# Performance work log

Hardware: AMD Instinct MI355X
Metric: run time of the kernel (lower is better)

## Reference

```python
import jax, jax.numpy as jnp
import numpy as np

B, P = 8, 768
S = 36                 # sample_points (also deformable offset pairs)
C_IN, C_ADJ = 64, 72   # prior_feat_channels -> adjusted channels
D, G = 512, 4          # fc_hidden_dim, num_groups (= attention heads)
N_OFFSETS, N_STRIPS, DEG = 72, 71, 3


def _bilinear(img, x, y):
    """img: [B,H,W,C]; x,y: [B,N] pixel coords. Bilinear sample, zeros outside."""
    H, W = img.shape[1], img.shape[2]
    x0 = jnp.floor(x); y0 = jnp.floor(y)
    x0i = x0.astype(jnp.int32); y0i = y0.astype(jnp.int32)
    wx1 = x - x0; wy1 = y - y0

    def corner(xi, yi, w):
        valid = (xi >= 0) & (xi < W) & (yi >= 0) & (yi < H)
        xc = jnp.clip(xi, 0, W - 1); yc = jnp.clip(yi, 0, H - 1)
        vals = jax.vmap(lambda f, yy, xx: f[yy, xx])(img, yc, xc)  # [B,N,C]
        return vals * (w * valid)[..., None]

    return (corner(x0i, y0i, (1 - wx1) * (1 - wy1))
            + corner(x0i + 1, y0i, wx1 * (1 - wy1))
            + corner(x0i, y0i + 1, (1 - wx1) * wy1)
            + corner(x0i + 1, y0i + 1, wx1 * wy1))


def _resize_ac(img, Ht, Wt):
    """Bilinear resize with align_corners=True. img: [B,H,W,C]."""
    Bsz, H, W, _ = img.shape
    gy, gx = jnp.meshgrid(jnp.linspace(0.0, H - 1.0, Ht),
                          jnp.linspace(0.0, W - 1.0, Wt), indexing='ij')
    xf = jnp.broadcast_to(gx.reshape(-1), (Bsz, Ht * Wt))
    yf = jnp.broadcast_to(gy.reshape(-1), (Bsz, Ht * Wt))
    return _bilinear(img, xf, yf).reshape(Bsz, Ht, Wt, -1)


def setup_inputs():
    ks = jax.random.split(jax.random.key(0), 32)
    r = lambda i, shp, s=1.0: jax.random.normal(ks[i], shp, dtype=jnp.float32) * s
    z = lambda shp: jnp.zeros(shp, jnp.float32)
    return {
        'feat0': r(0, (B, C_IN, 40, 100)),
        'feat1': r(1, (B, C_IN, 20, 50)),
        'feat2': r(2, (B, C_IN, 10, 25)),
        'priors': jax.random.uniform(ks[3], (B, P, 4 + N_OFFSETS), dtype=jnp.float32) * N_STRIPS,
        'ca_w': r(4, (C_ADJ, C_IN), 0.125), 'ca_b': z((C_ADJ,)),
        'off_w': r(5, (2 * S, C_ADJ), 0.01), 'off_b': r(6, (2 * S,), 0.01),
        'dp_w': r(7, (C_ADJ, C_ADJ), 0.167), 'dp_b': z((C_ADJ,)),
        'z_emb': r(8, (S,), 0.3) + 1.0,
        'gf_w': r(9, (D, S // G, C_ADJ), 0.02), 'gf_b': z((D,)),
        'wq': r(10, (D, D), 0.044), 'bq': z((D,)),
        'wk': r(11, (D, D), 0.044), 'bk': z((D,)),
        'wv': r(12, (D, D), 0.044), 'bv': z((D,)),
        'wo': r(13, (D, D), 0.044), 'bo': z((D,)),
        'cf_w1': r(14, (2 * D, D), 0.044), 'cf_b1': z((2 * D,)),
        'cf_w2': r(15, (D, 2 * D), 0.031), 'cf_b2': z((D,)),
        'cls_w1': r(16, (D, D), 0.044), 'cls_b1': z((D,)),
        'cls_w2': r(17, (2, D), 0.001), 'cls_b2': z((2,)),
        'reg_w1': r(18, (D, D), 0.044), 'reg_b1': z((D,)),
        'p_w1': r(19, (2 * D, D), 0.044), 'p_b1': z((2 * D,)),
        'p_w2': r(20, (DEG + 1, 2 * D), 0.031), 'p_b2': z((DEG + 1,)),
        'b_scale': jnp.ones((1,), jnp.float32), 'b_bias': z((1,)),
    }


def reference(feat0, feat1, feat2, priors, ca_w, ca_b, off_w, off_b, dp_w, dp_b,
              z_emb, gf_w, gf_b, wq, bq, wk, bk, wv, bv, wo, bo,
              cf_w1, cf_b1, cf_w2, cf_b2, cls_w1, cls_b1, cls_w2, cls_b2,
              reg_w1, reg_b1, p_w1, p_b1, p_w2, p_b2, b_scale, b_bias):
    f32 = jnp.float32
    lin = lambda x, w, b: x @ w.T + b

    # ---- prior sampling grid (CLRNet-style) ----
    sx_idx = jnp.floor(jnp.linspace(0.0, 1.0, S) * N_STRIPS).astype(jnp.int32)
    pf_ys = jnp.flip(1.0 - sx_idx.astype(f32) / N_STRIPS)            # [S]
    pf_xs = priors[..., 4 + sx_idx][:, :, ::-1]                       # [B,P,S]
    gx = jnp.clip(pf_xs / N_STRIPS, 0.0, 1.0) * 2.0 - 1.0            # [-1,1]
    gy = jnp.broadcast_to(pf_ys * 2.0 - 1.0, gx.shape)

    # ---- channel adjust (1x1 conv) per level, channels-last ----
    adj = lambda f: jnp.einsum('bchw,oc->bhwo', f, ca_w) + ca_b
    feats = [adj(feat0), adj(feat1), adj(feat2)]                      # [B,H,W,C_ADJ]
    offs0 = jnp.einsum('bhwc,oc->bhwo', feats[0], off_w) + off_b     # [B,H0,W0,2S]

    # ---- deformable multi-level sampling: per (prior, point) gather + 1x1 proj ----
    sidx = jnp.arange(S)
    levels = []
    for l, fl in enumerate(feats):
        Hl, Wl = fl.shape[1], fl.shape[2]
        offs = offs0 if l == 0 else _resize_ac(offs0, Hl, Wl)
        px = (gx + 1.0) * 0.5 * (Wl - 1)
        py = (gy + 1.0) * 0.5 * (Hl - 1)
        ov = _bilinear(offs, px.reshape(B, -1), py.reshape(B, -1)).reshape(B, P, S, S, 2)
        dyx = ov[:, :, sidx, sidx, :]                                 # offset pair s for point s
        sxp = (px + dyx[..., 1]).reshape(B, -1)
        syp = (py + dyx[..., 0]).reshape(B, -1)
        smp = _bilinear(fl, sxp, syp).reshape(B, P, S, C_ADJ)
        levels.append(smp @ dp_w.T + dp_b)
    feat_all = jnp.stack(levels)                                      # [3,B,P,S,C]

    # ---- z-embedding soft level selection ----
    zw = jax.nn.softmax(-(z_emb[:, None] - jnp.arange(3, dtype=f32)) ** 2 / 2.0, axis=-1)  # [S,3]
    feature = jnp.einsum('lbpsc,sl->bpsc', feat_all, zw)

    # ---- grouped gather Conv1d(S -> D, kernel=C_ADJ, groups=G) ----
    xg = feature.reshape(B * P, G, S // G, C_ADJ)
    wg = gf_w.reshape(G, D // G, S // G, C_ADJ)
    feature = (jnp.einsum('ngik,goik->ngo', xg, wg).reshape(B * P, D) + gf_b).reshape(B, P, D)

    # ---- multi-head self-attention over priors + channel MLP residual ----
    dh = D // G
    q = lin(feature, wq, bq).reshape(B, P, G, dh).transpose(0, 2, 1, 3)
    k = lin(feature, wk, bk).reshape(B, P, G, dh).transpose(0, 2, 1, 3)
    v = lin(feature, wv, bv).reshape(B, P, G, dh).transpose(0, 2, 1, 3)
    attn = jax.nn.softmax(jnp.einsum('bgqd,bgkd->bgqk', q, k) / float(np.sqrt(dh)), axis=-1)
    res = jnp.einsum('bgqk,bgkd->bgqd', attn, v).transpose(0, 2, 1, 3).reshape(B, P, D)
    res = lin(res, wo, bo)
    feature = feature + lin(jax.nn.relu(lin(res, cf_w1, cf_b1)), cf_w2, cf_b2)

    # ---- heads ----
    fc = feature.reshape(B * P, D)
    cls_logits = lin(jax.nn.relu(lin(fc, cls_w1, cls_b1)), cls_w2, cls_b2).reshape(B, P, 2)
    reg = jax.nn.relu(lin(fc, reg_w1, reg_b1)).reshape(B, P, D)
    coeffs = lin(jax.nn.relu(lin(reg, p_w1, p_b1)), p_w2, p_b2)       # [B,P,DEG+1]
    coeffs = jnp.concatenate([coeffs[..., :2], coeffs[..., 2:] * b_scale + b_bias], axis=-1)
    ys = jnp.linspace(0.0, 1.0, N_OFFSETS)
    basis = jnp.stack([ys ** i for i in range(DEG + 1)], axis=1)      # [N_OFFSETS, DEG+1]
    xs_pred = jax.nn.sigmoid(jnp.einsum('bnd,od->bno', coeffs, basis))
    return jnp.concatenate([cls_logits, coeffs, xs_pred], axis=-1)    # [B,P,78]
```

## Files before the change

kernel.cpp:

```cpp
#include <hip/hip_runtime.h>
#include <hip/hip_bf16.h>
#include <math.h>

#define BB 8
#define PP 768
#define NPRI 76
#define SS 36
#define CIN 64
#define CADJ 72
#define DD 512

#define H0 40
#define W0 100
#define H1 20
#define W1 50
#define H2 10
#define W2 25

typedef __attribute__((ext_vector_type(8))) short bf16x8;
typedef __attribute__((ext_vector_type(4))) short bf16x4;
typedef __attribute__((ext_vector_type(4))) float f32x4;
#define MFMA_BF16 __builtin_amdgcn_mfma_f32_16x16x32_bf16

typedef const __attribute__((address_space(1))) unsigned int* gas_t;
typedef __attribute__((address_space(3))) unsigned int* las_t;

__device__ __forceinline__ __hip_bfloat16 to_bf16(float v) { return __float2bfloat16(v); }
__device__ __forceinline__ float bf2f(__hip_bfloat16 v) { return __bfloat162float(v); }
__device__ __forceinline__ short to_bf16s(float v) {
    __hip_bfloat16 h = __float2bfloat16(v);
    return *reinterpret_cast<short*>(&h);
}
__device__ __forceinline__ float bfs2f(short s) {
    union { unsigned u; float f; } cv;
    cv.u = ((unsigned)(unsigned short)s) << 16;
    return cv.f;
}

__device__ __forceinline__ float bsample(const float* __restrict__ img, int H, int W,
                                         int C, int c, float x, float y)
{
    float x0f = floorf(x), y0f = floorf(y);
    int x0 = (int)x0f, y0 = (int)y0f;
    float wx1 = x - x0f, wy1 = y - y0f;
    float wx0 = 1.0f - wx1, wy0 = 1.0f - wy1;
    int xc0 = min(max(x0, 0), W - 1);
    int xc1 = min(max(x0 + 1, 0), W - 1);
    int yc0 = min(max(y0, 0), H - 1);
    int yc1 = min(max(y0 + 1, 0), H - 1);
    bool vx0 = (x0 >= 0) && (x0 < W);
    bool vx1 = (x0 + 1 >= 0) && (x0 + 1 < W);
    bool vy0 = (y0 >= 0) && (y0 < H);
    bool vy1 = (y0 + 1 >= 0) && (y0 + 1 < H);
    float w00 = (vx0 && vy0) ? wx0 * wy0 : 0.0f;
    float w01 = (vx1 && vy0) ? wx1 * wy0 : 0.0f;
    float w10 = (vx0 && vy1) ? wx0 * wy1 : 0.0f;
    float w11 = (vx1 && vy1) ? wx1 * wy1 : 0.0f;
    return w00 * img[((size_t)yc0 * W + xc0) * C + c]
         + w01 * img[((size_t)yc0 * W + xc1) * C + c]
         + w10 * img[((size_t)yc1 * W + xc0) * C + c]
         + w11 * img[((size_t)yc1 * W + xc1) * C + c];
}

__global__ __launch_bounds__(256) void k_wprep(
    const float* __restrict__ wq, const float* __restrict__ wk, const float* __restrict__ wv,
    const float* __restrict__ wo, const float* __restrict__ cf_w1, const float* __restrict__ cf_w2,
    const float* __restrict__ cls_w1, const float* __restrict__ reg_w1, const float* __restrict__ p_w1,
    const float* __restrict__ bq, const float* __restrict__ bk, const float* __restrict__ bv,
    const float* __restrict__ cls_b1, const float* __restrict__ reg_b1,
    const float* __restrict__ gf_w, const float* __restrict__ dp_w,
    const float* __restrict__ dp_b, const float* __restrict__ gf_b,
    __hip_bfloat16* __restrict__ wqkv, __hip_bfloat16* __restrict__ wo_bf,
    __hip_bfloat16* __restrict__ cf1_bf, __hip_bfloat16* __restrict__ cf2_bf,
    __hip_bfloat16* __restrict__ clsreg_bf, __hip_bfloat16* __restrict__ p1_bf,
    __hip_bfloat16* __restrict__ gfw2, float* __restrict__ b2,
    float* __restrict__ bqkv, float* __restrict__ bclsreg)
{
    __shared__ float dpS[CADJ][CADJ + 1];
    __shared__ float gfr[648];
    const int bid = blockIdx.x;
    const int tid = threadIdx.x;

    if (bid < 512) {
        const int o = bid;
        for (int i = tid; i < CADJ * CADJ; i += 256) dpS[i / CADJ][i % CADJ] = dp_w[i];
        for (int i = tid; i < 648; i += 256) gfr[i] = gf_w[(size_t)o * 648 + i];
        __syncthreads();
        for (int t = tid; t < 672; t += 256) {
            float acc = 0.0f;
            if (t < 648) {
                const int i = t / 72, m = t % 72;
                const float* gr = gfr + i * 72;
#pragma unroll 8
                for (int k = 0; k < 72; ++k) acc = fmaf(gr[k], dpS[k][m], acc);
            }
            gfw2[(size_t)o * 672 + t] = to_bf16(acc);
        }
        return;
    }
    if (bid < 514) {
        const int o = (bid - 512) * 256 + tid;
        if (o < DD) {
            const float* gr = gf_w + (size_t)o * 648;
            float acc = gf_b[o];
            for (int j = 0; j < 648; ++j) acc = fmaf(gr[j], dp_b[j % 72], acc);
            b2[o] = acc;
        }
        return;
    }
    long i = (long)(bid - 514) * 256 + tid;
    if (i < 262144) { wqkv[i] = to_bf16(wq[i]); return; }
    i -= 262144;
    if (i < 262144) { wqkv[262144 + i] = to_bf16(wk[i]); return; }
    i -= 262144;
    if (i < 262144) { wqkv[524288 + i] = to_bf16(wv[i]); return; }
    i -= 262144;
    if (i < 262144) { wo_bf[i] = to_bf16(wo[i]); return; }
    i -= 262144;
    if (i < 524288) { cf1_bf[i] = to_bf16(cf_w1[i]); return; }
    i -= 524288;
    if (i < 524288) { cf2_bf[i] = to_bf16(cf_w2[i]); return; }
    i -= 524288;
    if (i < 262144) { clsreg_bf[i] = to_bf16(cls_w1[i]); return; }
    i -= 262144;
    if (i < 262144) { clsreg_bf[262144 + i] = to_bf16(reg_w1[i]); return; }
    i -= 262144;
    if (i < 524288) { p1_bf[i] = to_bf16(p_w1[i]); return; }
    i -= 524288;
    if (i < 512) { bqkv[i] = bq[i]; return; }
    if (i < 1024) { bqkv[i] = bk[i - 512]; return; }
    if (i < 1536) { bqkv[i] = bv[i - 1024]; return; }
    i -= 1536;
    if (i < 512) { bclsreg[i] = cls_b1[i]; return; }
    if (i < 1024) { bclsreg[i] = reg_b1[i - 512]; return; }
}

__global__ __launch_bounds__(256) void k_adjoff(
    const float* __restrict__ f, const float* __restrict__ caw, const float* __restrict__ cab,
    const float* __restrict__ offw, const float* __restrict__ offb,
    __hip_bfloat16* __restrict__ feout, float* __restrict__ offout, int HW, int do_off)
{
    __shared__ float inS[64][65];
    __shared__ float wS[72][64];
    __shared__ float owS[72][73];
    __shared__ float feS[64][73];
    __shared__ float cabS[72], obS[72];

    const int tid = threadIdx.x;
    const int b = blockIdx.y;
    const int pix0 = blockIdx.x * 64;
    const int cnt = min(64, HW - pix0);
    const int px = tid & 63, og = tid >> 6, o0 = og * 18;

    const float* fb = f + (size_t)b * CIN * HW + pix0;
    for (int i = tid; i < 72 * 64; i += 256) wS[i >> 6][i & 63] = caw[i];
    if (do_off)
        for (int i = tid; i < 72 * 72; i += 256) owS[i / 72][i % 72] = offw[i];
    if (tid < 72) { cabS[tid] = cab[tid]; obS[tid] = do_off ? offb[tid] : 0.f; }
    for (int i = tid; i < 64 * 64; i += 256) {
        const int c = i >> 6, p = i & 63;
        inS[c][p] = (p < cnt) ? fb[(size_t)c * HW + p] : 0.f;
    }
    __syncthreads();

    float acc[18];
#pragma unroll
    for (int j = 0; j < 18; ++j) acc[j] = cabS[o0 + j];
#pragma unroll 4
    for (int c = 0; c < 64; ++c) {
        const float v = inS[c][px];
#pragma unroll
        for (int j = 0; j < 18; ++j) acc[j] = fmaf(v, wS[o0 + j][c], acc[j]);
    }
#pragma unroll
    for (int j = 0; j < 18; ++j) feS[px][o0 + j] = acc[j];
    __syncthreads();

    __hip_bfloat16* feg = feout + ((size_t)b * HW + pix0) * CADJ;
    for (int i = tid; i < cnt * CADJ; i += 256) feg[i] = to_bf16(feS[i / CADJ][i % CADJ]);

    if (!do_off) return;

    float acc2[18];
#pragma unroll
    for (int j = 0; j < 18; ++j) acc2[j] = obS[o0 + j];
#pragma unroll 4
    for (int c = 0; c < 72; ++c) {
        const float v = feS[px][c];
#pragma unroll
        for (int j = 0; j < 18; ++j) acc2[j] = fmaf(v, owS[o0 + j][c], acc2[j]);
    }
    __syncthreads();
#pragma unroll
    for (int j = 0; j < 18; ++j) feS[px][o0 + j] = acc2[j];
    __syncthreads();
    float* ofg = offout + ((size_t)b * HW + pix0) * CADJ;
    for (int i = tid; i < cnt * CADJ; i += 256) ofg[i] = feS[i / CADJ][i % CADJ];
}

__global__ __launch_bounds__(256) void k_adj12(
    const float* __restrict__ f1, const float* __restrict__ f2,
    const float* __restrict__ caw, const float* __restrict__ cab,
    __hip_bfloat16* __restrict__ fe1, __hip_bfloat16* __restrict__ fe2)
{
    __shared__ float inS[64][65];
    __shared__ float wS[72][64];
    __shared__ float feS[64][73];
    __shared__ float cabS[72];

    const int tid = threadIdx.x;
    const int b = blockIdx.y;
    const int bx = blockIdx.x;
    const float* f;
    __hip_bfloat16* fe;
    int HW, pix0;
    if (bx < 16) { f = f1; fe = fe1; HW = H1 * W1; pix0 = bx * 64; }
    else         { f = f2; fe = fe2; HW = H2 * W2; pix0 = (bx - 16) * 64; }
    const int cnt = min(64, HW - pix0);
    const int px = tid & 63, og = tid >> 6, o0 = og * 18;

    const float* fb = f + (size_t)b * CIN * HW + pix0;
    for (int i = tid; i < 72 * 64; i += 256) wS[i >> 6][i & 63] = caw[i];
    if (tid < 72) cabS[tid] = cab[tid];
    for (int i = tid; i < 64 * 64; i += 256) {
        const int c = i >> 6, p = i & 63;
        inS[c][p] = (p < cnt) ? fb[(size_t)c * HW + p] : 0.f;
    }
    __syncthreads();

    float acc[18];
#pragma unroll
    for (int j = 0; j < 18; ++j) acc[j] = cabS[o0 + j];
#pragma unroll 4
    for (int c = 0; c < 64; ++c) {
        const float v = inS[c][px];
#pragma unroll
        for (int j = 0; j < 18; ++j) acc[j] = fmaf(v, wS[o0 + j][c], acc[j]);
    }
#pragma unroll
    for (int j = 0; j < 18; ++j) feS[px][o0 + j] = acc[j];
    __syncthreads();

    __hip_bfloat16* feg = fe + ((size_t)b * HW + pix0) * CADJ;
    for (int i = tid; i < cnt * CADJ; i += 256) feg[i] = to_bf16(feS[i / CADJ][i % CADJ]);
}

__global__ __launch_bounds__(256) void k_resize2(const float* __restrict__ src,
    float* __restrict__ of1, float* __restrict__ of2)
{
    const int T1 = BB * H1 * W1 * CADJ;
    const int T2 = BB * H2 * W2 * CADJ;
    int idx = blockIdx.x * 256 + threadIdx.x;
    if (idx < T1) {
        const int c = idx % CADJ;
        const int j = (idx / CADJ) % W1;
        const int i = (idx / (CADJ * W1)) % H1;
        const int b = idx / (CADJ * W1 * H1);
        float sy = fminf((float)i * ((float)(H0 - 1) / (float)(H1 - 1)), (float)(H0 - 1));
        float sx = fminf((float)j * ((float)(W0 - 1) / (float)(W1 - 1)), (float)(W0 - 1));
        of1[idx] = bsample(src + (size_t)b * H0 * W0 * CADJ, H0, W0, CADJ, c, sx, sy);
        return;
    }
    idx -= T1;
    if (idx >= T2) return;
    const int c = idx % CADJ;
    const int j = (idx / CADJ) % W2;
    const int i = (idx / (CADJ * W2)) % H2;
    const int b = idx / (CADJ * W2 * H2);
    float sy = fminf((float)i * ((float)(H0 - 1) / (float)(H2 - 1)), (float)(H0 - 1));
    float sx = fminf((float)j * ((float)(W0 - 1) / (float)(W2 - 1)), (float)(W0 - 1));
    of2[idx] = bsample(src + (size_t)b * H0 * W0 * CADJ, H0, W0, CADJ, c, sx, sy);
}

__global__ __launch_bounds__(256) void k_sample(
    const float* __restrict__ priors,
    const __hip_bfloat16* __restrict__ feats0, const __hip_bfloat16* __restrict__ feats1,
    const __hip_bfloat16* __restrict__ feats2,
    const float* __restrict__ offs0,  const float* __restrict__ offs1,  const float* __restrict__ offs2,
    const float* __restrict__ z_emb,
    __hip_bfloat16* __restrict__ fsout)
{
    const int bid = blockIdx.x;
    const int gi = (bid & 7) * 384 + (bid >> 3);
    const int bp0 = gi * 2;
    const int b = bp0 / PP;
    const int tid = threadIdx.x;

    __shared__ __align__(16) int   ib[2][3][SS][4];
    __shared__ __align__(16) float wz[2][3][SS][4];

    const int Hs[3] = {H0, H1, H2};
    const int Wsz[3] = {W0, W1, W2};
    const __hip_bfloat16* Fb[3] = { feats0 + (size_t)b * H0 * W0 * CADJ,
                                    feats1 + (size_t)b * H1 * W1 * CADJ,
                                    feats2 + (size_t)b * H2 * W2 * CADJ };
    const float* Ob[3] = { offs0 + (size_t)b * H0 * W0 * CADJ,
                           offs1 + (size_t)b * H1 * W1 * CADJ,
                           offs2 + (size_t)b * H2 * W2 * CADJ };

    if (tid < 2 * 3 * SS) {
        const int p = tid / 108;
        const int l = (tid % 108) / SS;
        const int s = tid % SS;
        const int bp = bp0 + p;
        const float t = (float)(35 - s) / 35.0f;
        const int m = (int)floorf(t * 71.0f);
        const float pfx = priors[(size_t)bp * NPRI + 4 + m];
        const float gxv = fminf(fmaxf(pfx / 71.0f, 0.0f), 1.0f) * 2.0f - 1.0f;
        const float gyv = (1.0f - (float)m / 71.0f) * 2.0f - 1.0f;
        const float z = z_emb[s];
        const float e0 = expf(-0.5f * z * z);
        const float e1 = expf(-0.5f * (z - 1.0f) * (z - 1.0f));
        const float e2 = expf(-0.5f * (z - 2.0f) * (z - 2.0f));
        const float inv = 1.0f / (e0 + e1 + e2);
        const float ev[3] = {e0, e1, e2};
        const float zwl = ev[l] * inv;

        const int Hl = Hs[l], Wl = Wsz[l];
        const float px = (gxv + 1.0f) * 0.5f * (float)(Wl - 1);
        const float py = (gyv + 1.0f) * 0.5f * (float)(Hl - 1);
        const float dy = bsample(Ob[l], Hl, Wl, CADJ, 2 * s,     px, py);
        const float dx = bsample(Ob[l], Hl, Wl, CADJ, 2 * s + 1, px, py);
        const float sx = px + dx, sy = py + dy;
        const float x0f = floorf(sx), y0f = floorf(sy);
        const int x0 = (int)x0f, y0 = (int)y0f;
        const float wx1 = sx - x0f, wy1 = sy - y0f;
        const float wx0 = 1.0f - wx1, wy0 = 1.0f - wy1;
        const bool vx0 = (x0 >= 0) && (x0 < Wl);
        const bool vx1 = (x0 + 1 >= 0) && (x0 + 1 < Wl);
        const bool vy0 = (y0 >= 0) && (y0 < Hl);
        const bool vy1 = (y0 + 1 >= 0) && (y0 + 1 < Hl);
        const int xc0 = min(max(x0, 0), Wl - 1);
        const int xc1 = min(max(x0 + 1, 0), Wl - 1);
        const int yc0 = min(max(y0, 0), Hl - 1);
        const int yc1 = min(max(y0 + 1, 0), Hl - 1);
        wz[p][l][s][0] = ((vx0 && vy0) ? wx0 * wy0 : 0.0f) * zwl;
        wz[p][l][s][1] = ((vx1 && vy0) ? wx1 * wy0 : 0.0f) * zwl;
        wz[p][l][s][2] = ((vx0 && vy1) ? wx0 * wy1 : 0.0f) * zwl;
        wz[p][l][s][3] = ((vx1 && vy1) ? wx1 * wy1 : 0.0f) * zwl;
        ib[p][l][s][0] = (yc0 * Wl + xc0) * CADJ;
        ib[p][l][s][1] = (yc0 * Wl + xc1) * CADJ;
        ib[p][l][s][2] = (yc1 * Wl + xc0) * CADJ;
        ib[p][l][s][3] = (yc1 * Wl + xc1) * CADJ;
    }
    __syncthreads();

    for (int idx = tid; idx < 2 * SS * 18; idx += 256) {
        const int p = idx / 648;
        const int rem = idx % 648;
        const int s = rem / 18, k4 = (rem % 18) * 4;
        float a0 = 0.f, a1 = 0.f, a2 = 0.f, a3 = 0.f;
#pragma unroll
        for (int l = 0; l < 3; ++l) {
            const __hip_bfloat16* F = Fb[l];
            const int4   i4 = *(const int4*)&ib[p][l][s][0];
            const float4 w4 = *(const float4*)&wz[p][l][s][0];
            const bf16x4 v0 = *(const bf16x4*)(F + i4.x + k4);
            const bf16x4 v1 = *(const bf16x4*)(F + i4.y + k4);
            const bf16x4 v2 = *(const bf16x4*)(F + i4.z + k4);
            const bf16x4 v3 = *(const bf16x4*)(F + i4.w + k4);
            a0 = fmaf(w4.x, bfs2f(v0[0]), a0); a1 = fmaf(w4.x, bfs2f(v0[1]), a1);
            a2 = fmaf(w4.x, bfs2f(v0[2]), a2); a3 = fmaf(w4.x, bfs2f(v0[3]), a3);
            a0 = fmaf(w4.y, bfs2f(v1[0]), a0); a1 = fmaf(w4.y, bfs2f(v1[1]), a1);
            a2 = fmaf(w4.y, bfs2f(v1[2]), a2); a3 = fmaf(w4.y, bfs2f(v1[3]), a3);
            a0 = fmaf(w4.z, bfs2f(v2[0]), a0); a1 = fmaf(w4.z, bfs2f(v2[1]), a1);
            a2 = fmaf(w4.z, bfs2f(v2[2]), a2); a3 = fmaf(w4.z, bfs2f(v2[3]), a3);
            a0 = fmaf(w4.w, bfs2f(v3[0]), a0); a1 = fmaf(w4.w, bfs2f(v3[1]), a1);
            a2 = fmaf(w4.w, bfs2f(v3[2]), a2); a3 = fmaf(w4.w, bfs2f(v3[3]), a3);
        }
        bf16x4 pk;
        pk[0] = to_bf16s(a0); pk[1] = to_bf16s(a1);
        pk[2] = to_bf16s(a2); pk[3] = to_bf16s(a3);
        __hip_bfloat16* orow = fsout + (size_t)(bp0 + p) * 2688;
        *(bf16x4*)&orow[(s / 9) * 672 + (s % 9) * 72 + k4] = pk;
    }
    if (tid < 2 * 96) {
        const int p = tid / 96, g = (tid % 96) / 24, t = tid % 24;
        fsout[(size_t)(bp0 + p) * 2688 + g * 672 + 648 + t] = to_bf16(0.0f);
    }
}

__global__ __launch_bounds__(256) void k_bgemm(
    const __hip_bfloat16* __restrict__ A, int lda, long sAz,
    const __hip_bfloat16* __restrict__ W, int ldw, long sWz,
    const float* __restrict__ bias, int sBz,
    const __hip_bfloat16* __restrict__ Res, int ldres,
    __hip_bfloat16* __restrict__ C, int ldc, int sCz,
    int K, int relu)
{
    __shared__ __hip_bfloat16 As[2][128][32];
    __shared__ __hip_bfloat16 Bs[2][128][32];
    const int tid = threadIdx.x;
    const int lane = tid & 63, w = tid >> 6;
    const int wr = w >> 1, wc = w & 1;
    const int row16 = lane & 15, kg = lane >> 4;
    const int z = blockIdx.z;
    const int m0 = blockIdx.y * 128, n0 = blockIdx.x * 128;
    const __hip_bfloat16* Ab = A + (size_t)z * sAz;
    const __hip_bfloat16* Wb = W + (size_t)z * sWz;
    const int gr = lane >> 2;
    const int gc = (lane & 3) * 8;

#define STAGE128(buf, kbase)                                                       \
    {                                                                              \
        _Pragma("unroll")                                                          \
        for (int c = 0; c < 2; ++c) {                                              \
            const int r = w * 32 + c * 16;                                         \
            __builtin_amdgcn_global_load_lds(                                      \
                (gas_t)(Ab + (size_t)(m0 + r + gr) * lda + (kbase) + gc),          \
                (las_t)&As[buf][r][0], 16, 0, 0);                                  \
            __builtin_amdgcn_global_load_lds(                                      \
                (gas_t)(Wb + (size_t)(n0 + r + gr) * ldw + (kbase) + gc),          \
                (las_t)&Bs[buf][r][0], 16, 0, 0);                                  \
        }                                                                          \
    }

    f32x4 acc[4][4];
#pragma unroll
    for (int i = 0; i < 4; ++i)
#pragma unroll
        for (int j = 0; j < 4; ++j) acc[i][j] = (f32x4){0.f, 0.f, 0.f, 0.f};

    STAGE128(0, 0)
    __syncthreads();

    int cur = 0;
    for (int k0 = 0; k0 < K; k0 += 32) {
        if (k0 + 32 < K) STAGE128(cur ^ 1, k0 + 32)
        bf16x8 af[4], bfr[4];
#pragma unroll
        for (int i = 0; i < 4; ++i) af[i]  = *(const bf16x8*)&As[cur][wr * 64 + i * 16 + row16][kg * 8];
#pragma unroll
        for (int j = 0; j < 4; ++j) bfr[j] = *(const bf16x8*)&Bs[cur][wc * 64 + j * 16 + row16][kg * 8];
#pragma unroll
        for (int i = 0; i < 4; ++i)
#pragma unroll
            for (int j = 0; j < 4; ++j)
                acc[i][j] = MFMA_BF16(af[i], bfr[j], acc[i][j], 0, 0, 0);
        __syncthreads();
        cur ^= 1;
    }
#undef STAGE128

    const float* bz = bias + (size_t)z * sBz;
    __hip_bfloat16* Cz = C + (size_t)z * sCz;
#pragma unroll
    for (int i = 0; i < 4; ++i) {
#pragma unroll
        for (int r = 0; r < 4; ++r) {
            const int row = m0 + wr * 64 + i * 16 + kg * 4 + r;
#pragma unroll
            for (int j = 0; j < 4; ++j) {
                const int col = n0 + wc * 64 + j * 16 + row16;
                float v = acc[i][j][r] + bz[col];
                if (Res) v += bf2f(Res[(size_t)row * ldres + col]);
                if (relu) v = fmaxf(v, 0.0f);
                Cz[(size_t)row * ldc + col] = to_bf16(v);
            }
        }
    }
}

__global__ __launch_bounds__(256) void k_bgemm64(
    const __hip_bfloat16* __restrict__ A, int lda, long sAz,
    const __hip_bfloat16* __restrict__ W, int ldw, long sWz,
    const float* __restrict__ bias, int sBz,
    const __hip_bfloat16* __restrict__ Res, int ldres,
    __hip_bfloat16* __restrict__ C, int ldc, int sCz,
    int K, int relu)
{
    __shared__ __hip_bfloat16 As[2][64][32];
    __shared__ __hip_bfloat16 Bs[2][64][32];
    const int tid = threadIdx.x;
    const int lane = tid & 63, w = tid >> 6;
    const int wr = w >> 1, wc = w & 1;
    const int row16 = lane & 15, kg = lane >> 4;
    const int z = blockIdx.z;
    const int m0 = blockIdx.y * 64, n0 = blockIdx.x * 64;
    const __hip_bfloat16* Ab = A + (size_t)z * sAz;
    const __hip_bfloat16* Wb = W + (size_t)z * sWz;
    const int gr = lane >> 2;
    const int gc = (lane & 3) * 8;

    f32x4 acc[2][2];
#pragma unroll
    for (int i = 0; i < 2; ++i)
#pragma unroll
        for (int j = 0; j < 2; ++j) acc[i][j] = (f32x4){0.f, 0.f, 0.f, 0.f};

    __builtin_amdgcn_global_load_lds(
        (gas_t)(Ab + (size_t)(m0 + w * 16 + gr) * lda + gc),
        (las_t)&As[0][w * 16][0], 16, 0, 0);
    __builtin_amdgcn_global_load_lds(
        (gas_t)(Wb + (size_t)(n0 + w * 16 + gr) * ldw + gc),
        (las_t)&Bs[0][w * 16][0], 16, 0, 0);
    __syncthreads();

    int cur = 0;
    for (int k0 = 0; k0 < K; k0 += 32) {
        if (k0 + 32 < K) {
            const int nxt = cur ^ 1;
            __builtin_amdgcn_global_load_lds(
                (gas_t)(Ab + (size_t)(m0 + w * 16 + gr) * lda + k0 + 32 + gc),
                (las_t)&As[nxt][w * 16][0], 16, 0, 0);
            __builtin_amdgcn_global_load_lds(
                (gas_t)(Wb + (size_t)(n0 + w * 16 + gr) * ldw + k0 + 32 + gc),
                (las_t)&Bs[nxt][w * 16][0], 16, 0, 0);
        }
        bf16x8 af[2], bfr[2];
#pragma unroll
        for (int i = 0; i < 2; ++i) af[i]  = *(const bf16x8*)&As[cur][wr * 32 + i * 16 + row16][kg * 8];
#pragma unroll
        for (int j = 0; j < 2; ++j) bfr[j] = *(const bf16x8*)&Bs[cur][wc * 32 + j * 16 + row16][kg * 8];
#pragma unroll
        for (int i = 0; i < 2; ++i)
#pragma unroll
            for (int j = 0; j < 2; ++j)
                acc[i][j] = MFMA_BF16(af[i], bfr[j], acc[i][j], 0, 0, 0);
        __syncthreads();
        cur ^= 1;
    }

    const float* bz = bias + (size_t)z * sBz;
    __hip_bfloat16* Cz = C + (size_t)z * sCz;
#pragma unroll
    for (int i = 0; i < 2; ++i) {
#pragma unroll
        for (int r = 0; r < 4; ++r) {
            const int row = m0 + wr * 32 + i * 16 + kg * 4 + r;
#pragma unroll
            for (int j = 0; j < 2; ++j) {
                const int col = n0 + wc * 32 + j * 16 + row16;
                float v = acc[i][j][r] + bz[col];
                if (Res) v += bf2f(Res[(size_t)row * ldres + col]);
                if (relu) v = fmaxf(v, 0.0f);
                Cz[(size_t)row * ldc + col] = to_bf16(v);
            }
        }
    }
}

__global__ __launch_bounds__(256) void k_vt(
    const __hip_bfloat16* __restrict__ qkv, __hip_bfloat16* __restrict__ Vt)
{
    const int kt = blockIdx.x;
    const int bg = blockIdx.y;
    const int b = bg >> 2, g = bg & 3;
    const int tid = threadIdx.x;
    __shared__ unsigned short Vs[64][130];

    const __hip_bfloat16* src = qkv + (size_t)(b * PP + kt * 64) * 1536 + 1024 + g * 128;
    for (int i = tid; i < 1024; i += 256) {
        const int row = i >> 4, ch = i & 15;
        *(bf16x8*)&Vs[row][ch * 8] = *(const bf16x8*)(src + (size_t)row * 1536 + ch * 8);
    }
    __syncthreads();
    __hip_bfloat16* dst = Vt + (size_t)bg * 128 * 768 + kt * 64;
    for (int i = tid; i < 1024; i += 256) {
        const int d = i >> 3, kc = i & 7;
        bf16x8 pk;
#pragma unroll
        for (int j = 0; j < 8; ++j) pk[j] = (short)Vs[kc * 8 + j][d];
        *(bf16x8*)(dst + (size_t)d * 768 + kc * 8) = pk;
    }
}

__global__ __launch_bounds__(256) void k_fattn(
    const __hip_bfloat16* __restrict__ qkv, const __hip_bfloat16* __restrict__ Vt,
    __hip_bfloat16* __restrict__ Out)
{
    const int id = blockIdx.x;
    const int xcd = id & 7, rest = id >> 3;
    const int bg = xcd * 4 + rest / 12;
    const int qt = rest % 12;
    const int b = bg >> 2, g = bg & 3;
    const int tid = threadIdx.x, lane = tid & 63, w = tid >> 6;
    const int row16 = lane & 15, kg = lane >> 4;
    const int q0 = qt * 64;

    __shared__ __hip_bfloat16 Klds[64][136];
    __shared__ __hip_bfloat16 Vtl[128][72];
    __shared__ __hip_bfloat16 Plds[4][16][72];

    const size_t rowQ = (size_t)(b * PP + q0 + w * 16 + row16) * 1536 + g * 128;
    bf16x8 aq[4];
#pragma unroll
    for (int t = 0; t < 4; ++t)
        aq[t] = *(const bf16x8*)(qkv + rowQ + t * 32 + kg * 8);

    f32x4 oacc[8];
#pragma unroll
    for (int dt = 0; dt < 8; ++dt) oacc[dt] = (f32x4){0.f, 0.f, 0.f, 0.f};
    float mrow[4] = {-3.0e38f, -3.0e38f, -3.0e38f, -3.0e38f};
    float lrow[4] = {0.f, 0.f, 0.f, 0.f};

    const __hip_bfloat16* Kb = qkv + (size_t)(b * PP) * 1536 + 512 + g * 128;
    const __hip_bfloat16* Vb = Vt + (size_t)bg * 128 * 768;
    const float sc = 0.08838834764831845f;

    const int krow = tid >> 2, kch = tid & 3;
    const int vrow = tid >> 1, vch = tid & 1;
    bf16x8 kreg[4], vreg[4];

    {
        const __hip_bfloat16* s1 = Kb + (size_t)krow * 1536 + kch * 32;
        const __hip_bfloat16* s2 = Vb + (size_t)vrow * 768 + vch * 32;
#pragma unroll
        for (int j = 0; j < 4; ++j) { kreg[j] = *(const bf16x8*)(s1 + j * 8);
                                      vreg[j] = *(const bf16x8*)(s2 + j * 8); }
    }

    for (int kt = 0; kt < 12; ++kt) {
        __syncthreads();
#pragma unroll
        for (int j = 0; j < 4; ++j) {
            *(bf16x8*)&Klds[krow][kch * 32 + j * 8] = kreg[j];
            *(bf16x8*)&Vtl[vrow][vch * 32 + j * 8] = vreg[j];
        }
        __syncthreads();
        if (kt < 11) {
            const __hip_bfloat16* s1 = Kb + (size_t)((kt + 1) * 64 + krow) * 1536 + kch * 32;
            const __hip_bfloat16* s2 = Vb + (size_t)vrow * 768 + (kt + 1) * 64 + vch * 32;
#pragma unroll
            for (int j = 0; j < 4; ++j) { kreg[j] = *(const bf16x8*)(s1 + j * 8);
                                          vreg[j] = *(const bf16x8*)(s2 + j * 8); }
        }

        f32x4 s4[4];
#pragma unroll
        for (int st = 0; st < 4; ++st) s4[st] = (f32x4){0.f, 0.f, 0.f, 0.f};
        __builtin_amdgcn_s_setprio(1);
#pragma unroll
        for (int st = 0; st < 4; ++st)
#pragma unroll
            for (int t = 0; t < 4; ++t)
                s4[st] = MFMA_BF16(aq[t],
                    *(const bf16x8*)&Klds[st * 16 + row16][t * 32 + kg * 8], s4[st], 0, 0, 0);
        __builtin_amdgcn_s_setprio(0);

        float pm[4];
#pragma unroll
        for (int r = 0; r < 4; ++r) {
            float m0 = fmaxf(fmaxf(s4[0][r], s4[1][r]), fmaxf(s4[2][r], s4[3][r])) * sc;
            m0 = fmaxf(m0, __shfl_xor(m0, 1));
            m0 = fmaxf(m0, __shfl_xor(m0, 2));
            m0 = fmaxf(m0, __shfl_xor(m0, 4));
            m0 = fmaxf(m0, __shfl_xor(m0, 8));
            pm[r] = m0;
        }
        const float need = fmaxf(fmaxf(pm[0] - mrow[0], pm[1] - mrow[1]),
                                 fmaxf(pm[2] - mrow[2], pm[3] - mrow[3]));
        if (!__all(need <= 8.0f)) {
#pragma unroll
            for (int r = 0; r < 4; ++r) {
                const float mn = fmaxf(mrow[r], pm[r]);
                const float so = __expf(mrow[r] - mn);
                lrow[r] *= so;
#pragma unroll
                for (int dt = 0; dt < 8; ++dt) oacc[dt][r] *= so;
                mrow[r] = mn;
            }
        }
#pragma unroll
        for (int r = 0; r < 4; ++r) {
            float rs = 0.f;
#pragma unroll
            for (int st = 0; st < 4; ++st) {
                const float p = __expf(s4[st][r] * sc - mrow[r]);
                rs += p;
                Plds[w][kg * 4 + r][st * 16 + row16] = to_bf16(p);
            }
            rs += __shfl_xor(rs, 1);
            rs += __shfl_xor(rs, 2);
            rs += __shfl_xor(rs, 4);
            rs += __shfl_xor(rs, 8);
            lrow[r] += rs;
        }

        __builtin_amdgcn_s_setprio(1);
#pragma unroll
        for (int ks = 0; ks < 2; ++ks) {
            bf16x8 ap = *(const bf16x8*)&Plds[w][row16][ks * 32 + kg * 8];
#pragma unroll
            for (int dt = 0; dt < 8; ++dt)
                oacc[dt] = MFMA_BF16(ap,
                    *(const bf16x8*)&Vtl[dt * 16 + row16][ks * 32 + kg * 8], oacc[dt], 0, 0, 0);
        }
        __builtin_amdgcn_s_setprio(0);
    }

    const size_t obase = (size_t)(b * PP + q0 + w * 16 + kg * 4) * DD + g * 128;
#pragma unroll
    for (int r = 0; r < 4; ++r) {
        const float inv = 1.0f / lrow[r];
#pragma unroll
        for (int dt = 0; dt < 8; ++dt)
            Out[obase + (size_t)r * DD + dt * 16 + row16] = to_bf16(oacc[dt][r] * inv);
    }
}

__global__ __launch_bounds__(64) void k_head(
    const __hip_bfloat16* __restrict__ clsreg, const __hip_bfloat16* __restrict__ ph,
    const float* __restrict__ cls_w2, const float* __restrict__ cls_b2,
    const float* __restrict__ p_w2, const float* __restrict__ p_b2,
    const float* __restrict__ b_scale, const float* __restrict__ b_bias,
    float* __restrict__ outp)
{
    const int bp = blockIdx.x;
    const int lane = threadIdx.x;
    const __hip_bfloat16* hr = clsreg + (size_t)bp * 1024;
    float a0 = 0.0f, a1 = 0.0f;
    for (int i = lane; i < DD; i += 64) {
        float h = bf2f(hr[i]);
        a0 = fmaf(h, cls_w2[i], a0);
        a1 = fmaf(h, cls_w2[DD + i], a1);
    }
    const __hip_bfloat16* pr = ph + (size_t)bp * 1024;
    float c0 = 0.0f, c1 = 0.0f, c2 = 0.0f, c3 = 0.0f;
    for (int i = lane; i < 1024; i += 64) {
        float h = bf2f(pr[i]);
        c0 = fmaf(h, p_w2[i], c0);
        c1 = fmaf(h, p_w2[1024 + i], c1);
        c2 = fmaf(h, p_w2[2048 + i], c2);
        c3 = fmaf(h, p_w2[3072 + i], c3);
    }
#pragma unroll
    for (int off = 32; off > 0; off >>= 1) {
        a0 += __shfl_down(a0, off);
        a1 += __shfl_down(a1, off);
        c0 += __shfl_down(c0, off);
        c1 += __shfl_down(c1, off);
        c2 += __shfl_down(c2, off);
        c3 += __shfl_down(c3, off);
    }
    a0 = __shfl(a0, 0); a1 = __shfl(a1, 0);
    c0 = __shfl(c0, 0); c1 = __shfl(c1, 0);
    c2 = __shfl(c2, 0); c3 = __shfl(c3, 0);
    const float k0 = c0 + p_b2[0];
    const float k1 = c1 + p_b2[1];
    const float scv = b_scale[0], biv = b_bias[0];
    const float k2 = (c2 + p_b2[2]) * scv + biv;
    const float k3 = (c3 + p_b2[3]) * scv + biv;
    float* orow = outp + (size_t)bp * 78;
    if (lane == 0) {
        orow[0] = a0 + cls_b2[0];
        orow[1] = a1 + cls_b2[1];
        orow[2] = k0; orow[3] = k1; orow[4] = k2; orow[5] = k3;
    }
    for (int o = lane; o < 72; o += 64) {
        float ys = (float)o / 71.0f;
        float tv = k0 + ys * (k1 + ys * (k2 + ys * k3));
        orow[6 + o] = 1.0f / (1.0f + expf(-tv));
    }
}

extern "C" void kernel_launch(void* const* d_in, const int* in_sizes, int n_in,
                              void* d_out, int out_size, void* d_ws, size_t ws_size,
                              hipStream_t stream)
{
    const float* feat0  = (const float*)d_in[0];
    const float* feat1  = (const float*)d_in[1];
    const float* feat2  = (const float*)d_in[2];
    const float* priors = (const float*)d_in[3];
    const float* ca_w   = (const float*)d_in[4];
    const float* ca_b   = (const float*)d_in[5];
    const float* off_w  = (const float*)d_in[6];
    const float* off_b  = (const float*)d_in[7];
    const float* dp_w   = (const float*)d_in[8];
    const float* dp_b   = (const float*)d_in[9];
    const float* z_emb  = (const float*)d_in[10];
    const float* gf_w   = (const float*)d_in[11];
    const float* gf_b   = (const float*)d_in[12];
    const float* wq     = (const float*)d_in[13];
    const float* bq     = (const float*)d_in[14];
    const float* wk     = (const float*)d_in[15];
    const float* bk     = (const float*)d_in[16];
    const float* wv     = (const float*)d_in[17];
    const float* bv     = (const float*)d_in[18];
    const float* wo     = (const float*)d_in[19];
    const float* bo     = (const float*)d_in[20];
    const float* cf_w1  = (const float*)d_in[21];
    const float* cf_b1  = (const float*)d_in[22];
    const float* cf_w2  = (const float*)d_in[23];
    const float* cf_b2  = (const float*)d_in[24];
    const float* cls_w1 = (const float*)d_in[25];
    const float* cls_b1 = (const float*)d_in[26];
    const float* cls_w2 = (const float*)d_in[27];
    const float* cls_b2 = (const float*)d_in[28];
    const float* reg_w1 = (const float*)d_in[29];
    const float* reg_b1 = (const float*)d_in[30];
    const float* p_w1   = (const float*)d_in[31];
    const float* p_b1   = (const float*)d_in[32];
    const float* p_w2   = (const float*)d_in[33];
    const float* p_b2   = (const float*)d_in[34];
    const float* b_scale = (const float*)d_in[35];
    const float* b_bias  = (const float*)d_in[36];
    float* out = (float*)d_out;

    char* wsb = (char*)d_ws;
    __hip_bfloat16* feature = (__hip_bfloat16*)(wsb + 0);
    __hip_bfloat16* qkvb    = (__hip_bfloat16*)(wsb + 6291456);
    __hip_bfloat16* tb      = (__hip_bfloat16*)(wsb + 25165824);
    __hip_bfloat16* vtb     = (__hip_bfloat16*)(wsb + 31457280);
    __hip_bfloat16* rb      = (__hip_bfloat16*)(wsb + 31457280);
    __hip_bfloat16* hb      = (__hip_bfloat16*)(wsb + 37748736);
    __hip_bfloat16* f2      = (__hip_bfloat16*)(wsb + 50331648);
    __hip_bfloat16* clsregb = (__hip_bfloat16*)(wsb + 56623104);
    __hip_bfloat16* phb     = (__hip_bfloat16*)(wsb + 69206016);
    float* of1 = (float*)(wsb + 6291456);
    float* of2 = (float*)(wsb + 8595456);
    __hip_bfloat16* fe1 = (__hip_bfloat16*)(wsb + 9171456);
    __hip_bfloat16* fe2 = (__hip_bfloat16*)(wsb + 11475456);
    __hip_bfloat16* fsb = (__hip_bfloat16*)(wsb + 25165824);
    __hip_bfloat16* fe0 = (__hip_bfloat16*)(wsb + 58195968);
    float* of0 = (float*)(wsb + 67411968);
    __hip_bfloat16* wqkv_bf   = (__hip_bfloat16*)(wsb + 81788928);
    __hip_bfloat16* wo_bf     = (__hip_bfloat16*)(wsb + 83361792);
    __hip_bfloat16* cf1_bf    = (__hip_bfloat16*)(wsb + 83886080);
    __hip_bfloat16* cf2_bf    = (__hip_bfloat16*)(wsb + 84934656);
    __hip_bfloat16* clsreg_bf = (__hip_bfloat16*)(wsb + 85983232);
    __hip_bfloat16* p1_bf     = (__hip_bfloat16*)(wsb + 87031808);
    __hip_bfloat16* gfw2_bf   = (__hip_bfloat16*)(wsb + 88080384);
    float* bqkv    = (float*)(wsb + 88768512);
    float* bclsreg = (float*)(wsb + 88774656);
    float* b2      = (float*)(wsb + 88778752);

    k_wprep<<<12812, 256, 0, stream>>>(
        wq, wk, wv, wo, cf_w1, cf_w2, cls_w1, reg_w1, p_w1, bq, bk, bv, cls_b1, reg_b1,
        gf_w, dp_w, dp_b, gf_b,
        wqkv_bf, wo_bf, cf1_bf, cf2_bf, clsreg_bf, p1_bf, gfw2_bf, b2, bqkv, bclsreg);

    k_adjoff<<<dim3(63, BB), 256, 0, stream>>>(feat0, ca_w, ca_b, off_w, off_b,
                                               fe0, of0, H0 * W0, 1);
    k_adj12<<<dim3(20, BB), 256, 0, stream>>>(feat1, feat2, ca_w, ca_b, fe1, fe2);
    k_resize2<<<(BB * (H1 * W1 + H2 * W2) * CADJ + 255) / 256, 256, 0, stream>>>(of0, of1, of2);
    k_sample<<<3072, 256, 0, stream>>>(priors, fe0, fe1, fe2, of0, of1, of2, z_emb, fsb);

    const int M = BB * PP;
    k_bgemm64<<<dim3(2, M / 64, 4), 256, 0, stream>>>(
        fsb, 2688, 672, gfw2_bf, 672, 128 * 672, b2, 128,
        nullptr, 0, feature, DD, 128, 672, 0);
    k_bgemm<<<dim3(12, M / 128, 1), 256, 0, stream>>>(
        feature, DD, 0, wqkv_bf, DD, 0, bqkv, 0,
        nullptr, 0, qkvb, 1536, 0, DD, 0);
    k_vt<<<dim3(12, 32), 256, 0, stream>>>(qkvb, vtb);
    k_fattn<<<384, 256, 0, stream>>>(qkvb, vtb, tb);
    k_bgemm64<<<dim3(8, M / 64, 1), 256, 0, stream>>>(
        tb, DD, 0, wo_bf, DD, 0, bo, 0, nullptr, 0, rb, DD, 0, DD, 0);
    k_bgemm64<<<dim3(16, M / 64, 1), 256, 0, stream>>>(
        rb, DD, 0, cf1_bf, DD, 0, cf_b1, 0, nullptr, 0, hb, 1024, 0, DD, 1);
    k_bgemm64<<<dim3(8, M / 64, 1), 256, 0, stream>>>(
        hb, 1024, 0, cf2_bf, 1024, 0, cf_b2, 0, feature, DD, f2, DD, 0, 1024, 0);
    k_bgemm64<<<dim3(16, M / 64, 1), 256, 0, stream>>>(
        f2, DD, 0, clsreg_bf, DD, 0, bclsreg, 0, nullptr, 0, clsregb, 1024, 0, DD, 1);
    k_bgemm64<<<dim3(16, M / 64, 1), 256, 0, stream>>>(
        clsregb + 512, 1024, 0, p1_bf, DD, 0, p_b1, 0, nullptr, 0, phb, 1024, 0, DD, 1);

    k_head<<<M, 64, 0, stream>>>(clsregb, phb, cls_w2, cls_b2, p_w2, p_b2, b_scale, b_bias, out);
}
```

Measured before the change: 284.9 us.

## Vectorize weight casts, merge adj12 with resize, batch head and sample work

The weight-prep kernel now casts four floats per thread with float4 loads and packed bf16 stores, which cuts its grid about fourfold, and a single block copies the biases. The level-1/2 channel-adjust kernel and the offset resize kernel are merged into one launch. Each sample thread now handles both priors of a block, so index math is shared and more loads are in flight. The head kernel packs four rows per 256-thread block. The merge reads of0, written by an earlier launch on the same stream, so ordering is kept, but the cuts are mostly launch and overhead savings on small kernels.

```diff
diff --git a/kernel.cpp b/kernel.cpp
--- a/kernel.cpp
+++ b/kernel.cpp
@@ -62,6 +62,15 @@
          + w11 * img[((size_t)yc1 * W + xc1) * C + c];
 }
 
+__device__ __forceinline__ void cast4(__hip_bfloat16* dst, const float* src, long i)
+{
+    const float4 v = *(const float4*)(src + i * 4);
+    bf16x4 pk;
+    pk[0] = to_bf16s(v.x); pk[1] = to_bf16s(v.y);
+    pk[2] = to_bf16s(v.z); pk[3] = to_bf16s(v.w);
+    *(bf16x4*)(dst + i * 4) = pk;
+}
+
 __global__ __launch_bounds__(256) void k_wprep(
     const float* __restrict__ wq, const float* __restrict__ wk, const float* __restrict__ wv,
     const float* __restrict__ wo, const float* __restrict__ cf_w1, const float* __restrict__ cf_w2,
@@ -108,31 +117,34 @@
         }
         return;
     }
-    long i = (long)(bid - 514) * 256 + tid;
-    if (i < 262144) { wqkv[i] = to_bf16(wq[i]); return; }
-    i -= 262144;
-    if (i < 262144) { wqkv[262144 + i] = to_bf16(wk[i]); return; }
-    i -= 262144;
-    if (i < 262144) { wqkv[524288 + i] = to_bf16(wv[i]); return; }
-    i -= 262144;
-    if (i < 262144) { wo_bf[i] = to_bf16(wo[i]); return; }
-    i -= 262144;
-    if (i < 524288) { cf1_bf[i] = to_bf16(cf_w1[i]); return; }
-    i -= 524288;
-    if (i < 524288) { cf2_bf[i] = to_bf16(cf_w2[i]); return; }
-    i -= 524288;
-    if (i < 262144) { clsreg_bf[i] = to_bf16(cls_w1[i]); return; }
-    i -= 262144;
-    if (i < 262144) { clsreg_bf[262144 + i] = to_bf16(reg_w1[i]); return; }
-    i -= 262144;
-    if (i < 524288) { p1_bf[i] = to_bf16(p_w1[i]); return; }
-    i -= 524288;
-    if (i < 512) { bqkv[i] = bq[i]; return; }
-    if (i < 1024) { bqkv[i] = bk[i - 512]; return; }
-    if (i < 1536) { bqkv[i] = bv[i - 1024]; return; }
-    i -= 1536;
-    if (i < 512) { bclsreg[i] = cls_b1[i]; return; }
-    if (i < 1024) { bclsreg[i] = reg_b1[i - 512]; return; }
+    if (bid < 3586) {
+        long i = (long)(bid - 514) * 256 + tid;
+        if (i < 65536) { cast4(wqkv, wq, i); return; }
+        i -= 65536;
+        if (i < 65536) { cast4(wqkv + 262144, wk, i); return; }
+        i -= 65536;
+        if (i < 65536) { cast4(wqkv + 524288, wv, i); return; }
+        i -= 65536;
+        if (i < 65536) { cast4(wo_bf, wo, i); return; }
+        i -= 65536;
+        if (i < 131072) { cast4(cf1_bf, cf_w1, i); return; }
+        i -= 131072;
+        if (i < 131072) { cast4(cf2_bf, cf_w2, i); return; }
+        i -= 131072;
+        if (i < 65536) { cast4(clsreg_bf, cls_w1, i); return; }
+        i -= 65536;
+        if (i < 65536) { cast4(clsreg_bf + 262144, reg_w1, i); return; }
+        i -= 65536;
+        if (i < 131072) { cast4(p1_bf, p_w1, i); return; }
+        return;
+    }
+    for (int i = tid; i < 2560; i += 256) {
+        if (i < 512) bqkv[i] = bq[i];
+        else if (i < 1024) bqkv[i] = bk[i - 512];
+        else if (i < 1536) bqkv[i] = bv[i - 1024];
+        else if (i < 2048) bclsreg[i - 1536] = cls_b1[i - 1536];
+        else bclsreg[i - 1536] = reg_b1[i - 2048];
+    }
 }
 
 __global__ __launch_bounds__(256) void k_adjoff(
@@ -198,59 +210,61 @@
     for (int i = tid; i < cnt * CADJ; i += 256) ofg[i] = feS[i / CADJ][i % CADJ];
 }
 
-__global__ __launch_bounds__(256) void k_adj12(
+__global__ __launch_bounds__(256) void k_adjr12(
     const float* __restrict__ f1, const float* __restrict__ f2,
     const float* __restrict__ caw, const float* __restrict__ cab,
-    __hip_bfloat16* __restrict__ fe1, __hip_bfloat16* __restrict__ fe2)
-{
-    __shared__ float inS[64][65];
-    __shared__ float wS[72][64];
-    __shared__ float feS[64][73];
-    __shared__ float cabS[72];
-
+    __hip_bfloat16* __restrict__ fe1, __hip_bfloat16* __restrict__ fe2,
+    const float* __restrict__ of0, float* __restrict__ of1, float* __restrict__ of2)
+{
+    const int blk = blockIdx.x;
     const int tid = threadIdx.x;
-    const int b = blockIdx.y;
-    const int bx = blockIdx.x;
-    const float* f;
-    __hip_bfloat16* fe;
-    int HW, pix0;
-    if (bx < 16) { f = f1; fe = fe1; HW = H1 * W1; pix0 = bx * 64; }
-    else         { f = f2; fe = fe2; HW = H2 * W2; pix0 = (bx - 16) * 64; }
-    const int cnt = min(64, HW - pix0);
-    const int px = tid & 63, og = tid >> 6, o0 = og * 18;
-
-    const float* fb = f + (size_t)b * CIN * HW + pix0;
-    for (int i = tid; i < 72 * 64; i += 256) wS[i >> 6][i & 63] = caw[i];
-    if (tid < 72) cabS[tid] = cab[tid];
-    for (int i = tid; i < 64 * 64; i += 256) {
-        const int c = i >> 6, p = i & 63;
-        inS[c][p] = (p < cnt) ? fb[(size_t)c * HW + p] : 0.f;
-    }
-    __syncthreads();
-
-    float acc[18];
-#pragma unroll
-    for (int j = 0; j < 18; ++j) acc[j] = cabS[o0 + j];
+
+    if (blk < 160) {
+        __shared__ float inS[64][65];
+        __shared__ float wS[72][64];
+        __shared__ float feS[64][73];
+        __shared__ float cabS[72];
+
+        const int bx = blk % 20;
+        const int b = blk / 20;
+        const float* f;
+        __hip_bfloat16* fe;
+        int HW, pix0;
+        if (bx < 16) { f = f1; fe = fe1; HW = H1 * W1; pix0 = bx * 64; }
+        else         { f = f2; fe = fe2; HW = H2 * W2; pix0 = (bx - 16) * 64; }
+        const int cnt = min(64, HW - pix0);
+        const int px = tid & 63, og = tid >> 6, o0 = og * 18;
+
+        const float* fb = f + (size_t)b * CIN * HW + pix0;
+        for (int i = tid; i < 72 * 64; i += 256) wS[i >> 6][i & 63] = caw[i];
+        if (tid < 72) cabS[tid] = cab[tid];
+        for (int i = tid; i < 64 * 64; i += 256) {
+            const int c = i >> 6, p = i & 63;
+            inS[c][p] = (p < cnt) ? fb[(size_t)c * HW + p] : 0.f;
+        }
+        __syncthreads();
+
+        float acc[18];
+#pragma unroll
+        for (int j = 0; j < 18; ++j) acc[j] = cabS[o0 + j];
 #pragma unroll 4
-    for (int c = 0; c < 64; ++c) {
-        const float v = inS[c][px];
-#pragma unroll
-        for (int j = 0; j < 18; ++j) acc[j] = fmaf(v, wS[o0 + j][c], acc[j]);
-    }
-#pragma unroll
-    for (int j = 0; j < 18; ++j) feS[px][o0 + j] = acc[j];
-    __syncthreads();
-
-    __hip_bfloat16* feg = fe + ((size_t)b * HW + pix0) * CADJ;
-    for (int i = tid; i < cnt * CADJ; i += 256) feg[i] = to_bf16(feS[i / CADJ][i % CADJ]);
-}
-
-__global__ __launch_bounds__(256) void k_resize2(const float* __restrict__ src,
-    float* __restrict__ of1, float* __restrict__ of2)
-{
+        for (int c = 0; c < 64; ++c) {
+            const float v = inS[c][px];
+#pragma unroll
+            for (int j = 0; j < 18; ++j) acc[j] = fmaf(v, wS[o0 + j][c], acc[j]);
+        }
+#pragma unroll
+        for (int j = 0; j < 18; ++j) feS[px][o0 + j] = acc[j];
+        __syncthreads();
+
+        __hip_bfloat16* feg = fe + ((size_t)b * HW + pix0) * CADJ;
+        for (int i = tid; i < cnt * CADJ; i += 256) feg[i] = to_bf16(feS[i / CADJ][i % CADJ]);
+        return;
+    }
+
     const int T1 = BB * H1 * W1 * CADJ;
     const int T2 = BB * H2 * W2 * CADJ;
-    int idx = blockIdx.x * 256 + threadIdx.x;
+    int idx = (blk - 160) * 256 + tid;
     if (idx < T1) {
         const int c = idx % CADJ;
         const int j = (idx / CADJ) % W1;
@@ -258,7 +272,7 @@
         const int b = idx / (CADJ * W1 * H1);
         float sy = fminf((float)i * ((float)(H0 - 1) / (float)(H1 - 1)), (float)(H0 - 1));
         float sx = fminf((float)j * ((float)(W0 - 1) / (float)(W1 - 1)), (float)(W0 - 1));
-        of1[idx] = bsample(src + (size_t)b * H0 * W0 * CADJ, H0, W0, CADJ, c, sx, sy);
+        of1[idx] = bsample(of0 + (size_t)b * H0 * W0 * CADJ, H0, W0, CADJ, c, sx, sy);
         return;
     }
     idx -= T1;
@@ -269,7 +283,7 @@
     const int b = idx / (CADJ * W2 * H2);
     float sy = fminf((float)i * ((float)(H0 - 1) / (float)(H2 - 1)), (float)(H0 - 1));
     float sx = fminf((float)j * ((float)(W0 - 1) / (float)(W2 - 1)), (float)(W0 - 1));
-    of2[idx] = bsample(src + (size_t)b * H0 * W0 * CADJ, H0, W0, CADJ, c, sx, sy);
+    of2[idx] = bsample(of0 + (size_t)b * H0 * W0 * CADJ, H0, W0, CADJ, c, sx, sy);
 }
 
 __global__ __launch_bounds__(256) void k_sample(
@@ -345,34 +359,45 @@
     }
     __syncthreads();
 
-    for (int idx = tid; idx < 2 * SS * 18; idx += 256) {
-        const int p = idx / 648;
-        const int rem = idx % 648;
-        const int s = rem / 18, k4 = (rem % 18) * 4;
-        float a0 = 0.f, a1 = 0.f, a2 = 0.f, a3 = 0.f;
-#pragma unroll
-        for (int l = 0; l < 3; ++l) {
-            const __hip_bfloat16* F = Fb[l];
-            const int4   i4 = *(const int4*)&ib[p][l][s][0];
-            const float4 w4 = *(const float4*)&wz[p][l][s][0];
-            const bf16x4 v0 = *(const bf16x4*)(F + i4.x + k4);
-            const bf16x4 v1 = *(const bf16x4*)(F + i4.y + k4);
-            const bf16x4 v2 = *(const bf16x4*)(F + i4.z + k4);
-            const bf16x4 v3 = *(const bf16x4*)(F + i4.w + k4);
-            a0 = fmaf(w4.x, bfs2f(v0[0]), a0); a1 = fmaf(w4.x, bfs2f(v0[1]), a1);
-            a2 = fmaf(w4.x, bfs2f(v0[2]), a2); a3 = fmaf(w4.x, bfs2f(v0[3]), a3);
-            a0 = fmaf(w4.y, bfs2f(v1[0]), a0); a1 = fmaf(w4.y, bfs2f(v1[1]), a1);
-            a2 = fmaf(w4.y, bfs2f(v1[2]), a2); a3 = fmaf(w4.y, bfs2f(v1[3]), a3);
-            a0 = fmaf(w4.z, bfs2f(v2[0]), a0); a1 = fmaf(w4.z, bfs2f(v2[1]), a1);
-            a2 = fmaf(w4.z, bfs2f(v2[2]), a2); a3 = fmaf(w4.z, bfs2f(v2[3]), a3);
-            a0 = fmaf(w4.w, bfs2f(v3[0]), a0); a1 = fmaf(w4.w, bfs2f(v3[1]), a1);
-            a2 = fmaf(w4.w, bfs2f(v3[2]), a2); a3 = fmaf(w4.w, bfs2f(v3[3]), a3);
-        }
-        bf16x4 pk;
-        pk[0] = to_bf16s(a0); pk[1] = to_bf16s(a1);
-        pk[2] = to_bf16s(a2); pk[3] = to_bf16s(a3);
-        __hip_bfloat16* orow = fsout + (size_t)(bp0 + p) * 2688;
-        *(bf16x4*)&orow[(s / 9) * 672 + (s % 9) * 72 + k4] = pk;
+    for (int idx = tid; idx < SS * 18; idx += 256) {
+        const int s = idx / 18, k4 = (idx % 18) * 4;
+        float a[2][4] = {{0.f, 0.f, 0.f, 0.f}, {0.f, 0.f, 0.f, 0.f}};
+#pragma unroll
+        for (int p = 0; p < 2; ++p)
+#pragma unroll
+            for (int l = 0; l < 3; ++l) {
+                const __hip_bfloat16* F = Fb[l];
+                const int4   i4 = *(const int4*)&ib[p][l][s][0];
+                const float4 w4 = *(const float4*)&wz[p][l][s][0];
+                const bf16x4 v0 = *(const bf16x4*)(F + i4.x + k4);
+                const bf16x4 v1 = *(const bf16x4*)(F + i4.y + k4);
+                const bf16x4 v2 = *(const bf16x4*)(F + i4.z + k4);
+                const bf16x4 v3 = *(const bf16x4*)(F + i4.w + k4);
+                a[p][0] = fmaf(w4.x, bfs2f(v0[0]), a[p][0]);
+                a[p][1] = fmaf(w4.x, bfs2f(v0[1]), a[p][1]);
+                a[p][2] = fmaf(w4.x, bfs2f(v0[2]), a[p][2]);
+                a[p][3] = fmaf(w4.x, bfs2f(v0[3]), a[p][3]);
+                a[p][0] = fmaf(w4.y, bfs2f(v1[0]), a[p][0]);
+                a[p][1] = fmaf(w4.y, bfs2f(v1[1]), a[p][1]);
+                a[p][2] = fmaf(w4.y, bfs2f(v1[2]), a[p][2]);
+                a[p][3] = fmaf(w4.y, bfs2f(v1[3]), a[p][3]);
+                a[p][0] = fmaf(w4.z, bfs2f(v2[0]), a[p][0]);
+                a[p][1] = fmaf(w4.z, bfs2f(v2[1]), a[p][1]);
+                a[p][2] = fmaf(w4.z, bfs2f(v2[2]), a[p][2]);
+                a[p][3] = fmaf(w4.z, bfs2f(v2[3]), a[p][3]);
+                a[p][0] = fmaf(w4.w, bfs2f(v3[0]), a[p][0]);
+                a[p][1] = fmaf(w4.w, bfs2f(v3[1]), a[p][1]);
+                a[p][2] = fmaf(w4.w, bfs2f(v3[2]), a[p][2]);
+                a[p][3] = fmaf(w4.w, bfs2f(v3[3]), a[p][3]);
+            }
+        const int col = (s / 9) * 672 + (s % 9) * 72 + k4;
+#pragma unroll
+        for (int p = 0; p < 2; ++p) {
+            bf16x4 pk;
+            pk[0] = to_bf16s(a[p][0]); pk[1] = to_bf16s(a[p][1]);
+            pk[2] = to_bf16s(a[p][2]); pk[3] = to_bf16s(a[p][3]);
+            *(bf16x4*)&fsout[(size_t)(bp0 + p) * 2688 + col] = pk;
+        }
     }
     if (tid < 2 * 96) {
         const int p = tid / 96, g = (tid % 96) / 24, t = tid % 24;
@@ -699,15 +724,15 @@
     }
 }
 
-__global__ __launch_bounds__(64) void k_head(
+__global__ __launch_bounds__(256) void k_head(
     const __hip_bfloat16* __restrict__ clsreg, const __hip_bfloat16* __restrict__ ph,
     const float* __restrict__ cls_w2, const float* __restrict__ cls_b2,
     const float* __restrict__ p_w2, const float* __restrict__ p_b2,
     const float* __restrict__ b_scale, const float* __restrict__ b_bias,
     float* __restrict__ outp)
 {
-    const int bp = blockIdx.x;
-    const int lane = threadIdx.x;
+    const int bp = blockIdx.x * 4 + (threadIdx.x >> 6);
+    const int lane = threadIdx.x & 63;
     const __hip_bfloat16* hr = clsreg + (size_t)bp * 1024;
     float a0 = 0.0f, a1 = 0.0f;
     for (int i = lane; i < DD; i += 64) {
@@ -825,15 +850,15 @@
     float* bclsreg = (float*)(wsb + 88774656);
     float* b2      = (float*)(wsb + 88778752);
 
-    k_wprep<<<12812, 256, 0, stream>>>(
+    k_wprep<<<3587, 256, 0, stream>>>(
         wq, wk, wv, wo, cf_w1, cf_w2, cls_w1, reg_w1, p_w1, bq, bk, bv, cls_b1, reg_b1,
         gf_w, dp_w, dp_b, gf_b,
         wqkv_bf, wo_bf, cf1_bf, cf2_bf, clsreg_bf, p1_bf, gfw2_bf, b2, bqkv, bclsreg);
 
     k_adjoff<<<dim3(63, BB), 256, 0, stream>>>(feat0, ca_w, ca_b, off_w, off_b,
                                                fe0, of0, H0 * W0, 1);
-    k_adj12<<<dim3(20, BB), 256, 0, stream>>>(feat1, feat2, ca_w, ca_b, fe1, fe2);
-    k_resize2<<<(BB * (H1 * W1 + H2 * W2) * CADJ + 255) / 256, 256, 0, stream>>>(of0, of1, of2);
+    k_adjr12<<<160 + (BB * (H1 * W1 + H2 * W2) * CADJ + 255) / 256, 256, 0, stream>>>(
+        feat1, feat2, ca_w, ca_b, fe1, fe2, of0, of1, of2);
     k_sample<<<3072, 256, 0, stream>>>(priors, fe0, fe1, fe2, of0, of1, of2, z_emb, fsb);
 
     const int M = BB * PP;
@@ -856,5 +881,5 @@
     k_bgemm64<<<dim3(16, M / 64, 1), 256, 0, stream>>>(
         clsregb + 512, 1024, 0, p1_bf, DD, 0, p_b1, 0, nullptr, 0, phb, 1024, 0, DD, 1);
 
-    k_head<<<M, 64, 0, stream>>>(clsregb, phb, cls_w2, cls_b2, p_w2, p_b2, b_scale, b_bias, out);
-}
+    k_head<<<M / 4, 256, 0, stream>>>(clsregb, phb, cls_w2, cls_b2, p_w2, p_b2, b_scale, b_bias, out);
+}
```

Result: no change. 285.2 us (+0.1%).
